# Kernel tuning notes

Hardware: AMD Instinct MI355X
Metric: run time of the kernel (lower is better)

The kernel has to match this reference:

```python
import jax, jax.numpy as jnp
import numpy as np

B, T, D, H = 8, 1024, 512, 8
QD, PD, POSD, VD, K = 32, 4, 48, 64, 31
FF = 4 * D
FF1, FF2, FF3, NLA = FF * 3 // 4, FF, FF * 5 // 4, D * 3 // 4


def _swoosh_l(x):
    return jax.nn.softplus(x - 4.0) - 0.08 * x - 0.035


def _swoosh_r(x):
    return jax.nn.softplus(x - 1.0) - 0.08 * x - 0.313261687


def setup_inputs() -> dict:
    key = jax.random.key(0)
    ks = iter(jax.random.split(key, 64))

    def w(shape, fan_in):
        return jax.random.normal(next(ks), shape, jnp.float32) * (fan_in ** -0.5)

    inp = {
        'x': jax.random.normal(next(ks), (B, T, D), jnp.float32),
        'pos_emb': jax.random.normal(next(ks), (2 * T - 1, POSD), jnp.float32),
        'mask': jnp.ones((B, T), bool),
        'attw_q_w': w((D, H * QD), D), 'attw_k_w': w((D, H * QD), D),
        'attw_pq_w': w((D, H * PD), D), 'attw_pos_w': w((POSD, H * PD), POSD),
        'ff1_in_w': w((D, FF1), D), 'ff1_in_b': jnp.zeros(FF1),
        'ff1_out_w': w((FF1, D), FF1), 'ff1_out_b': jnp.zeros(D),
        'nla_w': w((D, NLA * 3), D), 'nla_b': jnp.zeros(NLA * 3),
        'nla_out_w': w((NLA, D), NLA), 'nla_out_b': jnp.zeros(D),
        'sa1_v_w': w((D, H * VD), D), 'sa1_v_b': jnp.zeros(H * VD),
        'sa1_o_w': w((H * VD, D), H * VD), 'sa1_o_b': jnp.zeros(D),
        'conv1_in_w': w((D, 2 * D), D), 'conv1_in_b': jnp.zeros(2 * D),
        'conv1_dw_w': w((D, 1, K), K), 'conv1_dw_b': jnp.zeros(D),
        'conv1_out_w': w((D, D), D), 'conv1_out_b': jnp.zeros(D),
        'ff2_in_w': w((D, FF2), D), 'ff2_in_b': jnp.zeros(FF2),
        'ff2_out_w': w((FF2, D), FF2), 'ff2_out_b': jnp.zeros(D),
        'mid_scale': jax.random.uniform(next(ks), (D,), jnp.float32),
        'sa2_v_w': w((D, H * VD), D), 'sa2_v_b': jnp.zeros(H * VD),
        'sa2_o_w': w((H * VD, D), H * VD), 'sa2_o_b': jnp.zeros(D),
        'conv2_in_w': w((D, 2 * D), D), 'conv2_in_b': jnp.zeros(2 * D),
        'conv2_dw_w': w((D, 1, K), K), 'conv2_dw_b': jnp.zeros(D),
        'conv2_out_w': w((D, D), D), 'conv2_out_b': jnp.zeros(D),
        'ff3_in_w': w((D, FF3), D), 'ff3_in_b': jnp.zeros(FF3),
        'ff3_out_w': w((FF3, D), FF3), 'ff3_out_b': jnp.zeros(D),
        'norm_bias': jnp.zeros(D), 'norm_log_scale': jnp.zeros(()),
        'out_scale': jax.random.uniform(next(ks), (D,), jnp.float32),
    }
    return inp


def _forward(x, pos_emb, attw_q_w, attw_k_w, attw_pq_w, attw_pos_w,
             ff1_in_w, ff1_in_b, ff1_out_w, ff1_out_b,
             nla_w, nla_b, nla_out_w, nla_out_b,
             sa1_v_w, sa1_v_b, sa1_o_w, sa1_o_b,
             conv1_in_w, conv1_in_b, conv1_dw_w, conv1_dw_b, conv1_out_w, conv1_out_b,
             ff2_in_w, ff2_in_b, ff2_out_w, ff2_out_b,
             mid_scale,
             sa2_v_w, sa2_v_b, sa2_o_w, sa2_o_b,
             conv2_in_w, conv2_in_b, conv2_dw_w, conv2_dw_b, conv2_out_w, conv2_out_b,
             ff3_in_w, ff3_in_b, ff3_out_w, ff3_out_b,
             norm_bias, norm_log_scale, out_scale, mask):
    res = x
    # --- relative-pos multi-head attention weights ---
    q = (x @ attw_q_w).reshape(B, T, H, QD).transpose(0, 2, 1, 3)
    k = (x @ attw_k_w).reshape(B, T, H, QD).transpose(0, 2, 1, 3)
    p = (x @ attw_pq_w).reshape(B, T, H, PD).transpose(0, 2, 1, 3)
    content = jnp.einsum('bhtd,bhsd->bhts', q, k) * (QD ** -0.5)
    rel = (pos_emb @ attw_pos_w).reshape(2 * T - 1, H, PD).transpose(1, 0, 2)
    idx = jnp.arange(T)[:, None] - jnp.arange(T)[None, :] + (T - 1)
    relg = rel[:, idx]  # [H, T, T, PD]
    scores = content + jnp.einsum('bhtd,htsd->bhts', p, relg)
    scores = jnp.where(mask[:, None, None, :], scores, -10000.0)
    attn = jax.nn.softmax(scores, axis=-1)
    attn = jnp.where(mask[:, None, :, None], attn, 0.0)

    def mk(y):
        return jnp.where(mask[..., None], y, 0.0)

    def ff(y, wi, bi, wo, bo):
        return _swoosh_l(y @ wi + bi) @ wo + bo

    def sa(y, vw, vb, ow, ob):
        v = (y @ vw + vb).reshape(B, T, H, VD).transpose(0, 2, 1, 3)
        o = jnp.einsum('bhts,bhsd->bhtd', attn, v).transpose(0, 2, 1, 3).reshape(B, T, H * VD)
        return o @ ow + ob

    def conv(y, iw, ib, dw, db, ow, ob):
        u = y @ iw + ib
        a, g = jnp.split(u, 2, axis=-1)
        a = (a * jax.nn.sigmoid(g)).transpose(0, 2, 1)  # [B, D, T]
        a = jnp.where(mask[:, None, :], a, 0.0)
        c = jax.lax.conv_general_dilated(a, dw, (1,), [(K // 2, K // 2)],
                                         dimension_numbers=('NCH', 'OIH', 'NCH'),
                                         feature_group_count=D) + db[None, :, None]
        c = _swoosh_r(c.transpose(0, 2, 1))
        return mk(c @ ow + ob)

    def bypass(r, u, s):
        s = jnp.clip(s, 0.2, 1.0)  # eval/steady regime
        return r + (u - r) * s

    x = mk(x + ff(x, ff1_in_w, ff1_in_b, ff1_out_w, ff1_out_b))
    # non-linear attention (uses head 0)
    a, b, c = jnp.split(x @ nla_w + nla_b, 3, axis=-1)
    att0 = jnp.einsum('bts,bsd->btd', attn[:, 0], jnp.tanh(b) * c)
    x = mk(x + ((a * att0) @ nla_out_w + nla_out_b))
    x = mk(x + sa(x, sa1_v_w, sa1_v_b, sa1_o_w, sa1_o_b))
    x = mk(x + conv(x, conv1_in_w, conv1_in_b, conv1_dw_w, conv1_dw_b, conv1_out_w, conv1_out_b))
    x = mk(x + ff(x, ff2_in_w, ff2_in_b, ff2_out_w, ff2_out_b))
    x = mk(bypass(res, x, mid_scale))
    x = mk(x + sa(x, sa2_v_w, sa2_v_b, sa2_o_w, sa2_o_b))
    x = mk(x + conv(x, conv2_in_w, conv2_in_b, conv2_dw_w, conv2_dw_b, conv2_out_w, conv2_out_b))
    x = mk(x + ff(x, ff3_in_w, ff3_in_b, ff3_out_w, ff3_out_b))
    # BiasNorm
    rms = jnp.sqrt(jnp.mean((x - norm_bias) ** 2, axis=-1, keepdims=True) + 1e-8)
    x = x / rms * jnp.exp(norm_log_scale)
    x = mk(bypass(res, x, out_scale))
    return x


def reference(x, pos_emb, mask, attw_q_w, attw_k_w, attw_pq_w, attw_pos_w,
              ff1_in_w, ff1_in_b, ff1_out_w, ff1_out_b,
              nla_w, nla_b, nla_out_w, nla_out_b,
              sa1_v_w, sa1_v_b, sa1_o_w, sa1_o_b,
              conv1_in_w, conv1_in_b, conv1_dw_w, conv1_dw_b, conv1_out_w, conv1_out_b,
              ff2_in_w, ff2_in_b, ff2_out_w, ff2_out_b,
              mid_scale,
              sa2_v_w, sa2_v_b, sa2_o_w, sa2_o_b,
              conv2_in_w, conv2_in_b, conv2_dw_w, conv2_dw_b, conv2_out_w, conv2_out_b,
              ff3_in_w, ff3_in_b, ff3_out_w, ff3_out_b,
              norm_bias, norm_log_scale, out_scale):
    return _forward(x, pos_emb, attw_q_w, attw_k_w, attw_pq_w, attw_pos_w,
                    ff1_in_w, ff1_in_b, ff1_out_w, ff1_out_b,
                    nla_w, nla_b, nla_out_w, nla_out_b,
                    sa1_v_w, sa1_v_b, sa1_o_w, sa1_o_b,
                    conv1_in_w, conv1_in_b, conv1_dw_w, conv1_dw_b, conv1_out_w, conv1_out_b,
                    ff2_in_w, ff2_in_b, ff2_out_w, ff2_out_b,
                    mid_scale,
                    sa2_v_w, sa2_v_b, sa2_o_w, sa2_o_b,
                    conv2_in_w, conv2_in_b, conv2_dw_w, conv2_dw_b, conv2_out_w, conv2_out_b,
                    ff3_in_w, ff3_in_b, ff3_out_w, ff3_out_b,
                    norm_bias, norm_log_scale, out_scale, mask)
```

## Files before the change

kernel.cpp:

```cpp
#include <hip/hip_runtime.h>
#include <hip/hip_bf16.h>
#include <math.h>

using bf16 = __hip_bfloat16;
using f16 = _Float16;
typedef short s16x8 __attribute__((ext_vector_type(8)));
typedef f16   f16x2 __attribute__((ext_vector_type(2)));
typedef float f32x4 __attribute__((ext_vector_type(4)));
typedef unsigned int u32;
#define DEV __device__ __forceinline__
#define AS1 __attribute__((address_space(1)))
#define AS3 __attribute__((address_space(3)))

constexpr int Bc = 8, Tc = 1024, Dc = 512, Hc = 8;
constexpr int QDc = 32, PDc = 4, POSDc = 48, VDc = 64;
constexpr int Nrow = Bc * Tc;
constexpr int KWc = 31;
constexpr float LOG2E = 1.4426950408889634f;

DEV float frcp(float x) { return __builtin_amdgcn_rcpf(x); }
DEV float softplus_f(float y) { return fmaxf(y, 0.f) + __logf(1.f + __expf(-fabsf(y))); }
DEV float swoosh_l_f(float x) { return softplus_f(x - 4.f) - 0.08f * x - 0.035f; }
DEV float swoosh_r_f(float x) { return softplus_f(x - 1.f) - 0.08f * x - 0.313261687f; }
DEV float sigmoid_f(float x)  { return frcp(1.f + __expf(-x)); }
DEV float tanh_f(float x) {
  float e = __expf(2.f * fminf(fmaxf(x, -15.f), 15.f));
  return (e - 1.f) * frcp(e + 1.f);
}
DEV float clip_s(float s)     { return fminf(fmaxf(s, 0.2f), 1.0f); }
DEV float to_f(bf16 x)  { return __bfloat162float(x); }
DEV float b2f(short s) { union { u32 u; float f; } z; z.u = (u32)(unsigned short)s << 16; return z.f; }
DEV short f2bb(float v) { bf16 h = __float2bfloat16(v); return *(short*)&h; }
DEV unsigned short f2h(float v) { f16 h = (f16)v; union { f16 x; unsigned short s; } z; z.x = h; return z.s; }
DEV float h2f(unsigned short s) { union { unsigned short s; f16 x; } z; z.s = s; return (float)z.x; }
DEV u32 packbf(float a, float b) {
  return ((u32)(unsigned short)f2bb(b) << 16) | (u32)(unsigned short)f2bb(a);
}
DEV float dot2(u32 a, u32 b, float c) {
#if __has_builtin(__builtin_amdgcn_fdot2)
  union { u32 u; f16x2 v; } x, y; x.u = a; y.u = b;
  return __builtin_amdgcn_fdot2(x.v, y.v, c, false);
#else
  return c + h2f(a & 0xffff) * h2f(b & 0xffff) + h2f(a >> 16) * h2f(b >> 16);
#endif
}

DEV float wave_sum(float v) {
#pragma unroll
  for (int o = 32; o > 0; o >>= 1) v += __shfl_xor(v, o);
  return v;
}

DEV void gload16(const void* g, void* l) {
  __builtin_amdgcn_global_load_lds((const AS1 u32*)g, (AS3 u32*)l, 16, 0, 0);
}

template <int ACT, int WM, int WN, int FM, int FN>
__global__ __launch_bounds__(256) void gemm_mfma(
    const bf16* __restrict__ A, const bf16* __restrict__ B,
    const float* __restrict__ bias, const float* __restrict__ resid,
    float* __restrict__ Cf, bf16* __restrict__ Cb, bf16* __restrict__ Cb2,
    const bf16* __restrict__ auxb, const float* __restrict__ auxf,
    const float* __restrict__ auxf2,
    int M, int N, int K, int lda, int ldb, int ldc,
    long sAz, long sBo, long sBi, long sCo, long sCi, int nh) {
  constexpr int BM = WM * FM * 16, BN = WN * FN * 16;
  constexpr int NPA = (ACT == 8) ? 3 : 1;
  constexpr int NPB = (ACT == 2) ? 2 : 1;
  constexpr int PANA = 384, PANB = 512;
  constexpr int ASZT = NPA * BM * 128;
  constexpr int BUF = (NPA * BM + NPB * BN) * 128;
  constexpr int LPS = NPA * (BM / 32) + NPB * (BN / 32);

  int z = blockIdx.z;
  int zo = z / nh, zi = z - zo * nh;
  A += (long)z * sAz;
  B += (long)zo * sBo + (long)zi * sBi;
  long coff = (long)zo * sCo + (long)zi * sCi;

  __shared__ char lds[2 * BUF];

  int tid = threadIdx.x;
  int lane = tid & 63, w = tid >> 6;
  int wm = w / WN, wn = w % WN;

  int gx = gridDim.x;
  int nwg = gx * gridDim.y;
  int flat = blockIdx.y * gx + blockIdx.x;
  if ((nwg & 7) == 0) flat = (flat & 7) * (nwg >> 3) + (flat >> 3);
  int m0 = (flat / gx) * BM, n0 = (flat % gx) * BN;

  int lrow = lane >> 3, lch = lane & 7;
  const bf16* ga = A + (long)(m0 + w * (BM / 4) + lrow) * lda + ((lch ^ lrow) << 3);
  const bf16* gb = B + (long)(n0 + w * (BN / 4) + lrow) * ldb + ((lch ^ lrow) << 3);

  f32x4 acc[NPA * NPB][FM][FN];
#pragma unroll
  for (int p = 0; p < NPA * NPB; ++p)
#pragma unroll
    for (int i = 0; i < FM; ++i)
#pragma unroll
      for (int j = 0; j < FN; ++j) acc[p][i][j] = 0.f;

  int nt = K >> 6;
  {
#pragma unroll
    for (int pa = 0; pa < NPA; ++pa) {
      const bf16* gp = ga + (long)(pa * PANA) * lda;
      char* la = lds + pa * BM * 128 + w * (BM / 4) * 128;
#pragma unroll
      for (int i = 0; i < BM / 32; ++i) gload16(gp + (long)(i * 8) * lda, la + i * 1024);
    }
#pragma unroll
    for (int pb = 0; pb < NPB; ++pb) {
      const bf16* gp = gb + (long)(pb * PANB) * ldb;
      char* lb = lds + ASZT + pb * BN * 128 + w * (BN / 4) * 128;
#pragma unroll
      for (int i = 0; i < BN / 32; ++i) gload16(gp + (long)(i * 8) * ldb, lb + i * 1024);
    }
  }

  for (int t = 0; t < nt; ++t) {
    char* cA = lds + (t & 1) * BUF;
    if (t + 1 < nt) {
      int k0 = (t + 1) << 6;
      char* base = lds + ((t + 1) & 1) * BUF;
#pragma unroll
      for (int pa = 0; pa < NPA; ++pa) {
        const bf16* gp = ga + (long)(pa * PANA) * lda + k0;
        char* la = base + pa * BM * 128 + w * (BM / 4) * 128;
#pragma unroll
        for (int i = 0; i < BM / 32; ++i) gload16(gp + (long)(i * 8) * lda, la + i * 1024);
      }
#pragma unroll
      for (int pb = 0; pb < NPB; ++pb) {
        const bf16* gp = gb + (long)(pb * PANB) * ldb + k0;
        char* lb = base + ASZT + pb * BN * 128 + w * (BN / 4) * 128;
#pragma unroll
        for (int i = 0; i < BN / 32; ++i) gload16(gp + (long)(i * 8) * ldb, lb + i * 1024);
      }
      asm volatile("s_waitcnt vmcnt(%0)" :: "n"(LPS) : "memory");
    } else {
      asm volatile("s_waitcnt vmcnt(0)" ::: "memory");
    }
    __builtin_amdgcn_s_barrier();
    __builtin_amdgcn_sched_barrier(0);
#pragma unroll
    for (int ks = 0; ks < 2; ++ks) {
      int cg = ks * 4 + (lane >> 4);
      s16x8 af[NPA][FM], bfr[NPB][FN];
#pragma unroll
      for (int pa = 0; pa < NPA; ++pa)
#pragma unroll
        for (int f = 0; f < FM; ++f) {
          int row = wm * FM * 16 + f * 16 + (lane & 15);
          af[pa][f] = *(const s16x8*)(cA + pa * BM * 128 + row * 128 +
                                      ((cg ^ (row & 7)) << 4));
        }
#pragma unroll
      for (int pb = 0; pb < NPB; ++pb)
#pragma unroll
        for (int f = 0; f < FN; ++f) {
          int row = wn * FN * 16 + f * 16 + (lane & 15);
          bfr[pb][f] = *(const s16x8*)(cA + ASZT + pb * BN * 128 + row * 128 +
                                       ((cg ^ (row & 7)) << 4));
        }
#pragma unroll
      for (int pa = 0; pa < NPA; ++pa)
#pragma unroll
        for (int pb = 0; pb < NPB; ++pb)
#pragma unroll
          for (int fm = 0; fm < FM; ++fm)
#pragma unroll
            for (int fn = 0; fn < FN; ++fn)
              acc[pa * NPB + pb][fm][fn] = __builtin_amdgcn_mfma_f32_16x16x32_bf16(
                  af[pa][fm], bfr[pb][fn], acc[pa * NPB + pb][fm][fn], 0, 0, 0);
    }
    __builtin_amdgcn_sched_barrier(0);
    __builtin_amdgcn_s_barrier();
  }

  int rbase = m0 + wm * FM * 16 + (lane >> 4) * 4;
  int cbase = n0 + wn * FN * 16 + (lane & 15);
#pragma unroll
  for (int fn = 0; fn < FN; ++fn) {
    int col = cbase + fn * 16;
    if (col >= N) continue;
#pragma unroll
    for (int fm = 0; fm < FM; ++fm) {
#pragma unroll
      for (int r = 0; r < 4; ++r) {
        int row = rbase + fm * 16 + r;
        if (row >= M) continue;
        long ci = coff + (long)row * ldc + col;
        if constexpr (ACT == 2) {
          float va = acc[0][fm][fn][r] + bias[col];
          float vg = acc[1][fm][fn][r] + bias[col + 512];
          Cb[ci] = __float2bfloat16(va * sigmoid_f(vg));
        } else if constexpr (ACT == 4) {
          float a = to_f(auxb[(long)col * 8192 + (long)zo * 1024 + row]);
          Cb[ci] = __float2bfloat16(acc[0][fm][fn][r] * a);
        } else if constexpr (ACT == 5) {
          float v = acc[0][fm][fn][r] + bias[col] + resid[ci];
          float rv = auxf[ci];
          float o = rv + (v - rv) * clip_s(auxf2[col]);
          Cf[ci] = o;
          Cb[ci] = __float2bfloat16(o);
        } else if constexpr (ACT == 7) {
          Cb[ci] = __float2bfloat16(acc[0][fm][fn][r] + bias[row]);
        } else if constexpr (ACT == 8) {
          float va = acc[0][fm][fn][r] + bias[row];
          float vb = acc[1][fm][fn][r] + bias[row + 384];
          float vc = acc[2][fm][fn][r] + bias[row + 768];
          Cb2[ci] = __float2bfloat16(va);
          Cb[ci] = __float2bfloat16(tanh_f(vb) * vc);
        } else if constexpr (ACT == 9) {
          float v = acc[0][fm][fn][r];
          if (col < 512) {
            Cb2[(long)row * 512 + col] = __float2bfloat16(v);
          } else {
            Cb[(long)row * ldc + (col - 512)] =
                __float2bfloat16(swoosh_l_f(v + bias[col - 512]));
          }
        } else {
          float v = acc[0][fm][fn][r] + (bias ? bias[col] : 0.f);
          if (ACT == 1) v = swoosh_l_f(v);
          if (resid) v += resid[ci];
          if (Cf) Cf[ci] = v;
          if (Cb) Cb[ci] = __float2bfloat16(v);
        }
      }
    }
  }
}

__global__ __launch_bounds__(256) void relph_kernel(
    const float* __restrict__ pos_emb, const float* __restrict__ Wpos,
    float* __restrict__ relb,
    const float* __restrict__ x0, const float* __restrict__ Wpq,
    f16* __restrict__ ph) {
  int zz = blockIdx.z;
  const float* A  = zz ? x0 : pos_emb;
  const float* Bm = zz ? Wpq : Wpos;
  int M = zz ? Nrow : (2 * Tc - 1);
  int K = zz ? Dc : POSDc;
  int lda = K;
  int m0 = blockIdx.y * 64;
  if (m0 >= M) return;

  __shared__ float As[16][72];
  __shared__ float Bs[16][72];
  int tid = threadIdx.x;
  int tx = tid & 15, ty = tid >> 4;
  int arow = tid >> 2, ak4 = (tid & 3) * 4;
  int bk = tid >> 4, bn4 = (tid & 15) * 4;
  float acc[4][4] = {};
  for (int k0 = 0; k0 < K; k0 += 16) {
    int gm = m0 + arow;
#pragma unroll
    for (int j = 0; j < 4; ++j) {
      int gk = k0 + ak4 + j;
      As[ak4 + j][arow] = (gm < M && gk < K) ? A[(long)gm * lda + gk] : 0.f;
    }
    int gk = k0 + bk;
#pragma unroll
    for (int j = 0; j < 4; ++j) {
      int gn = bn4 + j;
      Bs[bk][bn4 + j] = (gk < K && gn < 32) ? Bm[(long)gk * 32 + gn] : 0.f;
    }
    __syncthreads();
#pragma unroll
    for (int kk = 0; kk < 16; ++kk) {
      float a4[4], b4[4];
#pragma unroll
      for (int i = 0; i < 4; ++i) a4[i] = As[kk][ty * 4 + i];
#pragma unroll
      for (int i = 0; i < 4; ++i) b4[i] = Bs[kk][tx * 4 + i];
#pragma unroll
      for (int i = 0; i < 4; ++i)
#pragma unroll
        for (int j = 0; j < 4; ++j) acc[i][j] += a4[i] * b4[j];
    }
    __syncthreads();
  }
#pragma unroll
  for (int i = 0; i < 4; ++i) {
    int gm = m0 + ty * 4 + i;
    if (gm >= M) continue;
#pragma unroll
    for (int j = 0; j < 4; ++j) {
      int gn = tx * 4 + j;
      if (gn < 32) {
        if (zz) ph[(long)gm * 32 + gn] = (f16)(acc[i][j] * LOG2E);
        else    relb[(long)gm * 32 + gn] = acc[i][j];
      }
    }
  }
}

struct TDesc { const float* src; bf16* dst; int K, N, tile0, ntx; float scale; };
struct TBatch { TDesc d[18]; int n; };

__global__ __launch_bounds__(256) void transpose_batch_kernel(TBatch tb) {
  int tile = blockIdx.x;
  int wi = 0;
#pragma unroll 1
  for (int i = 1; i < 18; ++i)
    if (i < tb.n && tb.d[i].tile0 <= tile) wi = i;
  const float* W = tb.d[wi].src;
  bf16* WT = tb.d[wi].dst;
  int K = tb.d[wi].K, N = tb.d[wi].N;
  float sc = tb.d[wi].scale;
  int lt = tile - tb.d[wi].tile0;
  int ntx = tb.d[wi].ntx;
  int bx = (lt % ntx) * 32, by = (lt / ntx) * 32;

  __shared__ float t[32][33];
  int lx = threadIdx.x & 31, ly = threadIdx.x >> 5;
#pragma unroll
  for (int j = 0; j < 4; ++j) {
    int k = by + ly + j * 8, n = bx + lx;
    if (k < K && n < N) t[ly + j * 8][lx] = W[(long)k * N + n];
  }
  __syncthreads();
#pragma unroll
  for (int j = 0; j < 4; ++j) {
    int n = bx + ly + j * 8, k = by + lx;
    if (n < N && k < K) WT[(long)n * K + k] = __float2bfloat16(t[lx][ly + j * 8] * sc);
  }
}

__global__ void dw_transpose_kernel(const float* __restrict__ dw1, float* __restrict__ o1,
                                    const float* __restrict__ dw2, float* __restrict__ o2) {
  int i = blockIdx.x * 256 + threadIdx.x;
  if (i >= 2 * 512 * KWc) return;
  const float* s = (i < 512 * KWc) ? dw1 : dw2;
  float* o = (i < 512 * KWc) ? o1 : o2;
  int j = (i < 512 * KWc) ? i : i - 512 * KWc;
  int d = j / KWc, kk = j - d * KWc;
  o[kk * 512 + d] = s[j];
}

__global__ void f2b_kernel(const float* __restrict__ in, bf16* __restrict__ out, int nOct) {
  int i = blockIdx.x * 256 + threadIdx.x;
  if (i >= nOct) return;
  float4 a = *(const float4*)(in + (long)i * 8);
  float4 b = *(const float4*)(in + (long)i * 8 + 4);
  s16x8 o;
  o[0] = f2bb(a.x); o[1] = f2bb(a.y); o[2] = f2bb(a.z); o[3] = f2bb(a.w);
  o[4] = f2bb(b.x); o[5] = f2bb(b.y); o[6] = f2bb(b.z); o[7] = f2bb(b.w);
  *(s16x8*)((short*)out + (long)i * 8) = o;
}

__global__ __launch_bounds__(256) void scores_softmax_fused(
    const bf16* __restrict__ qk, const f16* __restrict__ ph,
    const float* __restrict__ rel, bf16* __restrict__ attn) {
  int bh = blockIdx.y;
  int h = bh & (Hc - 1), b = bh >> 3;
  int t0 = blockIdx.x * 16;
  int tid = threadIdx.x, lane = tid & 63, w = tid >> 6;

  __shared__ unsigned short eS[16 * 1024];
  __shared__ u32 rel01[1040], rel23[1040];
  __shared__ u32 pS[16][2];
  __shared__ float lS[16][4];

  for (int i = tid; i < 1039; i += 256) {
    float4 rv = *(const float4*)(rel + (long)(t0 + i) * 32 + h * 4);
    rel01[i] = ((u32)f2h(rv.y) << 16) | f2h(rv.x);
    rel23[i] = ((u32)f2h(rv.w) << 16) | f2h(rv.z);
  }
  if (tid < 16) {
    const u32* pp = (const u32*)(ph + ((long)(b * Tc + t0 + tid)) * 32 + h * 4);
    pS[tid][0] = pp[0]; pS[tid][1] = pp[1];
  }
  __syncthreads();

  s16x8 af = *(const s16x8*)(qk + ((long)(b * Tc + t0 + (lane & 15))) * 512 +
                             h * QDc + (lane >> 4) * 8);
  int g = lane >> 4;
  u32 p01[4], p23[4];
#pragma unroll
  for (int r = 0; r < 4; ++r) { p01[r] = pS[g * 4 + r][0]; p23[r] = pS[g * 4 + r][1]; }
  float sum[4] = {0.f, 0.f, 0.f, 0.f};
  f32x4 zero = {0.f, 0.f, 0.f, 0.f};
  int cols0 = w * 256;
#pragma unroll 4
  for (int tile = 0; tile < 16; ++tile) {
    int s0 = cols0 + tile * 16;
    s16x8 bfr = *(const s16x8*)(qk + ((long)(b * Tc + s0 + (lane & 15))) * 512 +
                                256 + h * QDc + (lane >> 4) * 8);
    f32x4 acc = __builtin_amdgcn_mfma_f32_16x16x32_bf16(af, bfr, zero, 0, 0, 0);
    int scol = s0 + (lane & 15);
    int idx0 = g * 4 - scol + 1023;
#pragma unroll
    for (int r = 0; r < 4; ++r) {
      int idx = idx0 + r;
      float pos = dot2(p23[r], rel23[idx], dot2(p01[r], rel01[idx], 0.f));
      float e = exp2f(acc[r] + pos);
      sum[r] += e;
      *(unsigned short*)((char*)eS + (g * 4 + r) * 2048 + ((scol * 2) ^ (g << 5))) =
          (unsigned short)f2bb(e);
    }
  }
#pragma unroll
  for (int o = 1; o < 16; o <<= 1)
#pragma unroll
    for (int r = 0; r < 4; ++r) sum[r] += __shfl_xor(sum[r], o);
  if ((lane & 15) == 0) {
#pragma unroll
    for (int r = 0; r < 4; ++r) lS[g * 4 + r][w] = sum[r];
  }
  __syncthreads();

#pragma unroll
  for (int rr = 0; rr < 4; ++rr) {
    int row = w * 4 + rr;
    float inv = frcp(lS[row][0] + lS[row][1] + lS[row][2] + lS[row][3]);
    int mask = ((row >> 2) & 3) << 5;
    char* rowbase = (char*)eS + row * 2048;
    u32* grow = (u32*)(attn + ((long)bh * Tc + t0 + row) * Tc);
#pragma unroll
    for (int k = 0; k < 8; ++k) {
      u32 ew = *(u32*)(rowbase + (((lane + k * 64) * 4) ^ mask));
      grow[lane + k * 64] = packbf(b2f((short)(ew & 0xffff)) * inv,
                                   b2f((short)(ew >> 16)) * inv);
    }
  }
}

__global__ __launch_bounds__(256) void dwconv_kernel(
    const bf16* __restrict__ a, const float* __restrict__ dwT,
    const float* __restrict__ db, bf16* __restrict__ c) {
  int i = blockIdx.x * 256 + threadIdx.x;
  int oct = i & 63, bt = i >> 6;
  int t = bt & (Tc - 1), b0 = bt - t;
  float acc0 = db[oct * 8 + 0], acc1 = db[oct * 8 + 1], acc2 = db[oct * 8 + 2],
        acc3 = db[oct * 8 + 3], acc4 = db[oct * 8 + 4], acc5 = db[oct * 8 + 5],
        acc6 = db[oct * 8 + 6], acc7 = db[oct * 8 + 7];
#pragma unroll
  for (int kk = 0; kk < KWc; ++kk) {
    int tt = t + kk - (KWc / 2);
    if ((unsigned)tt < (unsigned)Tc) {
      s16x8 av = *(const s16x8*)((const short*)a + ((long)(b0 + tt) << 9) + oct * 8);
      const float* wp = dwT + kk * 512 + oct * 8;
      float4 w0 = *(const float4*)wp, w1 = *(const float4*)(wp + 4);
      acc0 += b2f(av[0]) * w0.x; acc1 += b2f(av[1]) * w0.y;
      acc2 += b2f(av[2]) * w0.z; acc3 += b2f(av[3]) * w0.w;
      acc4 += b2f(av[4]) * w1.x; acc5 += b2f(av[5]) * w1.y;
      acc6 += b2f(av[6]) * w1.z; acc7 += b2f(av[7]) * w1.w;
    }
  }
  s16x8 o;
  o[0] = f2bb(swoosh_r_f(acc0)); o[1] = f2bb(swoosh_r_f(acc1));
  o[2] = f2bb(swoosh_r_f(acc2)); o[3] = f2bb(swoosh_r_f(acc3));
  o[4] = f2bb(swoosh_r_f(acc4)); o[5] = f2bb(swoosh_r_f(acc5));
  o[6] = f2bb(swoosh_r_f(acc6)); o[7] = f2bb(swoosh_r_f(acc7));
  *(s16x8*)((short*)c + (long)bt * 512 + oct * 8) = o;
}

__global__ __launch_bounds__(256) void rmsnorm_bypass_kernel(
    const float* __restrict__ x, const float* __restrict__ x0,
    const float* __restrict__ nb, const float* __restrict__ nls,
    const float* __restrict__ os, float* __restrict__ out) {
  int row = blockIdx.x;
  int tid = threadIdx.x;
  const float* xr = x + (long)row * 512;
  const float* rr = x0 + (long)row * 512;
  float* orow = out + (long)row * 512;
  float v0 = xr[tid], v1 = xr[tid + 256];
  float d0 = v0 - nb[tid], d1 = v1 - nb[tid + 256];
  float ss = d0 * d0 + d1 * d1;
  __shared__ float red[4];
  int lane = tid & 63, wid = tid >> 6;
  ss = wave_sum(ss);
  if (lane == 0) red[wid] = ss;
  __syncthreads();
  ss = red[0] + red[1] + red[2] + red[3];
  float rms = sqrtf(ss * (1.f / 512.f) + 1e-8f);
  float scl = expf(nls[0]) / rms;
  float r0 = rr[tid], s0 = clip_s(os[tid]);
  orow[tid] = r0 + (v0 * scl - r0) * s0;
  float r1 = rr[tid + 256], s1 = clip_s(os[tid + 256]);
  orow[tid + 256] = r1 + (v1 * scl - r1) * s1;
}

static inline int cdiv(int a, int b) { return (a + b - 1) / b; }

template <int ACT, int WM = 2, int WN = 2, int FM = 2, int FN = 2>
static void mfma_launch(hipStream_t st, const bf16* A, const bf16* B, const float* bias,
                        const float* resid, float* Cf, bf16* Cb, bf16* Cb2,
                        const bf16* auxb, const float* auxf, const float* auxf2,
                        int M, int N, int K, int lda, int ldb, int ldc,
                        int Z = 1, int nh = 1, long sAz = 0, long sBo = 0, long sBi = 0,
                        long sCo = 0, long sCi = 0) {
  dim3 grid(cdiv(N, WN * FN * 16), cdiv(M, WM * FM * 16), Z);
  gemm_mfma<ACT, WM, WN, FM, FN><<<grid, dim3(256), 0, st>>>(
      A, B, bias, resid, Cf, Cb, Cb2, auxb, auxf, auxf2, M, N, K, lda, ldb, ldc,
      sAz, sBo, sBi, sCo, sCi, nh);
}
#define MFMA_AV 4, 1, 2, 4

extern "C" void kernel_launch(void* const* d_in, const int* in_sizes, int n_in,
                              void* d_out, int out_size, void* d_ws, size_t ws_size,
                              hipStream_t stream) {
  const float* x0        = (const float*)d_in[0];
  const float* pos_emb   = (const float*)d_in[1];
  const float* Wq        = (const float*)d_in[3];
  const float* Wk        = (const float*)d_in[4];
  const float* Wpq       = (const float*)d_in[5];
  const float* Wpos      = (const float*)d_in[6];
  const float* ff1_in_w  = (const float*)d_in[7];
  const float* ff1_in_b  = (const float*)d_in[8];
  const float* ff1_out_w = (const float*)d_in[9];
  const float* ff1_out_b = (const float*)d_in[10];
  const float* nla_w     = (const float*)d_in[11];
  const float* nla_b     = (const float*)d_in[12];
  const float* nla_out_w = (const float*)d_in[13];
  const float* nla_out_b = (const float*)d_in[14];
  const float* sa1_v_w   = (const float*)d_in[15];
  const float* sa1_v_b   = (const float*)d_in[16];
  const float* sa1_o_w   = (const float*)d_in[17];
  const float* sa1_o_b   = (const float*)d_in[18];
  const float* cv1_in_w  = (const float*)d_in[19];
  const float* cv1_in_b  = (const float*)d_in[20];
  const float* cv1_dw_w  = (const float*)d_in[21];
  const float* cv1_dw_b  = (const float*)d_in[22];
  const float* cv1_out_w = (const float*)d_in[23];
  const float* cv1_out_b = (const float*)d_in[24];
  const float* ff2_in_w  = (const float*)d_in[25];
  const float* ff2_in_b  = (const float*)d_in[26];
  const float* ff2_out_w = (const float*)d_in[27];
  const float* ff2_out_b = (const float*)d_in[28];
  const float* mid_scale = (const float*)d_in[29];
  const float* sa2_v_w   = (const float*)d_in[30];
  const float* sa2_v_b   = (const float*)d_in[31];
  const float* sa2_o_w   = (const float*)d_in[32];
  const float* sa2_o_b   = (const float*)d_in[33];
  const float* cv2_in_w  = (const float*)d_in[34];
  const float* cv2_in_b  = (const float*)d_in[35];
  const float* cv2_dw_w  = (const float*)d_in[36];
  const float* cv2_dw_b  = (const float*)d_in[37];
  const float* cv2_out_w = (const float*)d_in[38];
  const float* cv2_out_b = (const float*)d_in[39];
  const float* ff3_in_w  = (const float*)d_in[40];
  const float* ff3_in_b  = (const float*)d_in[41];
  const float* ff3_out_w = (const float*)d_in[42];
  const float* ff3_out_b = (const float*)d_in[43];
  const float* norm_bias = (const float*)d_in[44];
  const float* nls       = (const float*)d_in[45];
  const float* out_scale = (const float*)d_in[46];
  float* out = (float*)d_out;

  char* wsb = (char*)d_ws;
  size_t off = 0;
  bf16* attn  = (bf16*)(wsb + off); off += (size_t)Bc * Hc * Tc * Tc * 2;
  float* xA   = (float*)(wsb + off); off += (size_t)Nrow * Dc * 4;
  float* xB   = (float*)(wsb + off); off += (size_t)Nrow * Dc * 4;
  bf16*  xb   = (bf16*)(wsb + off);  off += (size_t)Nrow * Dc * 2;
  bf16*  x0b  = (bf16*)(wsb + off);  off += (size_t)Nrow * Dc * 2;
  bf16*  big1b = (bf16*)(wsb + off); off += (size_t)Nrow * 2560 * 2;
  bf16*  big2b = (bf16*)(wsb + off); off += (size_t)Nrow * Dc * 2;
  bf16*  wT    = (bf16*)(wsb + off); off += (size_t)9961472 * 2;
  float* dwT1  = (float*)(wsb + off); off += (size_t)KWc * 512 * 4;
  float* dwT2  = (float*)(wsb + off); off += (size_t)KWc * 512 * 4;
  bf16*  tbcT  = (bf16*)(wsb + off); off += (size_t)384 * Nrow * 2;
  bf16* big3b = big1b + (size_t)Nrow * 2048;
  bf16* vT    = big2b;
  bf16* qkb   = big2b;
  bf16* aT    = big1b;
  f16*  ph    = (f16*)(big1b + (size_t)Nrow * 1536);
  float* relb = (float*)(ph + (size_t)Nrow * 32);

  bf16* p_w = wT;
  auto alloc_w = [&](int n, int k) { bf16* r = p_w; p_w += (size_t)n * k; return r; };
  bf16* qkff1_wT   = alloc_w(2048, 512);
  bf16* ff1_out_wT = alloc_w(512, 1536);
  bf16* nla_wT     = alloc_w(1152, 512);
  bf16* nla_out_wT = alloc_w(512, 384);
  bf16* sa1_v_wT   = alloc_w(512, 512);
  bf16* sa1_o_wT   = alloc_w(512, 512);
  bf16* cv1_in_wT  = alloc_w(1024, 512);
  bf16* cv1_out_wT = alloc_w(512, 512);
  bf16* ff2_in_wT  = alloc_w(2048, 512);
  bf16* ff2_out_wT = alloc_w(512, 2048);
  bf16* sa2_v_wT   = alloc_w(512, 512);
  bf16* sa2_o_wT   = alloc_w(512, 512);
  bf16* cv2_in_wT  = alloc_w(1024, 512);
  bf16* cv2_out_wT = alloc_w(512, 512);
  bf16* ff3_in_wT  = alloc_w(2560, 512);
  bf16* ff3_out_wT = alloc_w(512, 2560);

  const int nOctD = Nrow * 64;

  f2b_kernel<<<cdiv(nOctD, 256), 256, 0, stream>>>(x0, x0b, nOctD);
  {
    TBatch tb{};
    auto add = [&](int idx, const float* s, bf16* d, int K, int N, int& t0, float sc) {
      tb.d[idx] = {s, d, K, N, t0, cdiv(N, 32), sc};
      t0 += cdiv(N, 32) * cdiv(K, 32);
    };
    int t0 = 0;
    add(0,  Wq,        qkff1_wT,   512, 256,  t0, 0.17677669529663687f * LOG2E);
    add(1,  Wk,        qkff1_wT + (size_t)256 * 512, 512, 256, t0, 1.f);
    add(2,  ff1_in_w,  qkff1_wT + (size_t)512 * 512, 512, 1536, t0, 1.f);
    add(3,  ff1_out_w, ff1_out_wT, 1536, 512, t0, 1.f);
    add(4,  nla_w,     nla_wT,     512, 1152, t0, 1.f);
    add(5,  nla_out_w, nla_out_wT, 384, 512,  t0, 1.f);
    add(6,  sa1_v_w,   sa1_v_wT,   512, 512,  t0, 1.f);
    add(7,  sa1_o_w,   sa1_o_wT,   512, 512,  t0, 1.f);
    add(8,  cv1_in_w,  cv1_in_wT,  512, 1024, t0, 1.f);
    add(9,  cv1_out_w, cv1_out_wT, 512, 512,  t0, 1.f);
    add(10, ff2_in_w,  ff2_in_wT,  512, 2048, t0, 1.f);
    add(11, ff2_out_w, ff2_out_wT, 2048, 512, t0, 1.f);
    add(12, sa2_v_w,   sa2_v_wT,   512, 512,  t0, 1.f);
    add(13, sa2_o_w,   sa2_o_wT,   512, 512,  t0, 1.f);
    add(14, cv2_in_w,  cv2_in_wT,  512, 1024, t0, 1.f);
    add(15, cv2_out_w, cv2_out_wT, 512, 512,  t0, 1.f);
    add(16, ff3_in_w,  ff3_in_wT,  512, 2560, t0, 1.f);
    add(17, ff3_out_w, ff3_out_wT, 2560, 512, t0, 1.f);
    tb.n = 18;
    transpose_batch_kernel<<<t0, 256, 0, stream>>>(tb);
  }
  dw_transpose_kernel<<<cdiv(2 * 512 * KWc, 256), 256, 0, stream>>>(
      cv1_dw_w, dwT1, cv2_dw_w, dwT2);
  relph_kernel<<<dim3(1, 128, 2), 256, 0, stream>>>(pos_emb, Wpos, relb, x0, Wpq, ph);

  mfma_launch<9>(stream, x0b, qkff1_wT, ff1_in_b, nullptr, nullptr, big1b, qkb,
                 nullptr, nullptr, nullptr, Nrow, 2048, 512, 512, 512, 1536);
  scores_softmax_fused<<<dim3(Tc / 16, 64), 256, 0, stream>>>(qkb, ph, relb, attn);

  mfma_launch<0>(stream, big1b, ff1_out_wT, ff1_out_b, x0, xA, xb, nullptr,
                 nullptr, nullptr, nullptr, Nrow, 512, 1536, 1536, 1536, 512);

  mfma_launch<8>(stream, nla_wT, xb, nla_b, nullptr, nullptr, tbcT, aT,
                 nullptr, nullptr, nullptr, 384, Nrow, 512, 512, 512, Nrow);
  mfma_launch<4>(stream, attn, tbcT, nullptr, nullptr, nullptr, big3b, nullptr,
                 aT, nullptr, nullptr, Tc, 384, Tc, Tc, Nrow, 384,
                 Bc, 1, (long)Hc * Tc * Tc, 1024, 0, (long)Tc * 384, 0);
  mfma_launch<0>(stream, big3b, nla_out_wT, nla_out_b, xA, xB, xb, nullptr,
                 nullptr, nullptr, nullptr, Nrow, 512, 384, 384, 384, 512);

  mfma_launch<7>(stream, sa1_v_wT, xb, sa1_v_b, nullptr, nullptr, vT, nullptr,
                 nullptr, nullptr, nullptr, 512, Nrow, 512, 512, 512, Nrow);
  mfma_launch<0, MFMA_AV>(stream, attn, vT, nullptr, nullptr, nullptr, big3b, nullptr,
                          nullptr, nullptr, nullptr, Tc, VDc, Tc, Tc, Nrow, 512,
                          Bc * Hc, Hc, (long)Tc * Tc, Tc, (long)VDc * Nrow,
                          (long)Tc * 512, VDc);
  mfma_launch<0>(stream, big3b, sa1_o_wT, sa1_o_b, xB, xA, xb, nullptr,
                 nullptr, nullptr, nullptr, Nrow, 512, 512, 512, 512, 512);

  mfma_launch<2>(stream, xb, cv1_in_wT, cv1_in_b, nullptr, nullptr, big2b, nullptr,
                 nullptr, nullptr, nullptr, Nrow, 512, 512, 512, 512, 512);
  dwconv_kernel<<<cdiv(nOctD, 256), 256, 0, stream>>>(big2b, dwT1, cv1_dw_b, big3b);
  mfma_launch<0>(stream, big3b, cv1_out_wT, cv1_out_b, xA, xB, xb, nullptr,
                 nullptr, nullptr, nullptr, Nrow, 512, 512, 512, 512, 512);

  mfma_launch<1>(stream, xb, ff2_in_wT, ff2_in_b, nullptr, nullptr, big1b, nullptr,
                 nullptr, nullptr, nullptr, Nrow, 2048, 512, 512, 512, 2048);
  mfma_launch<5>(stream, big1b, ff2_out_wT, ff2_out_b, xB, xB, xb, nullptr,
                 nullptr, x0, mid_scale, Nrow, 512, 2048, 2048, 2048, 512);

  mfma_launch<7>(stream, sa2_v_wT, xb, sa2_v_b, nullptr, nullptr, vT, nullptr,
                 nullptr, nullptr, nullptr, 512, Nrow, 512, 512, 512, Nrow);
  mfma_launch<0, MFMA_AV>(stream, attn, vT, nullptr, nullptr, nullptr, big3b, nullptr,
                          nullptr, nullptr, nullptr, Tc, VDc, Tc, Tc, Nrow, 512,
                          Bc * Hc, Hc, (long)Tc * Tc, Tc, (long)VDc * Nrow,
                          (long)Tc * 512, VDc);
  mfma_launch<0>(stream, big3b, sa2_o_wT, sa2_o_b, xB, xA, xb, nullptr,
                 nullptr, nullptr, nullptr, Nrow, 512, 512, 512, 512, 512);

  mfma_launch<2>(stream, xb, cv2_in_wT, cv2_in_b, nullptr, nullptr, big2b, nullptr,
                 nullptr, nullptr, nullptr, Nrow, 512, 512, 512, 512, 512);
  dwconv_kernel<<<cdiv(nOctD, 256), 256, 0, stream>>>(big2b, dwT2, cv2_dw_b, big3b);
  mfma_launch<0>(stream, big3b, cv2_out_wT, cv2_out_b, xA, xB, xb, nullptr,
                 nullptr, nullptr, nullptr, Nrow, 512, 512, 512, 512, 512);

  mfma_launch<1>(stream, xb, ff3_in_wT, ff3_in_b, nullptr, nullptr, big1b, nullptr,
                 nullptr, nullptr, nullptr, Nrow, 2560, 512, 512, 512, 2560);
  mfma_launch<0>(stream, big1b, ff3_out_wT, ff3_out_b, xB, xA, nullptr, nullptr,
                 nullptr, nullptr, nullptr, Nrow, 512, 2560, 2560, 2560, 512);

  rmsnorm_bypass_kernel<<<Nrow, 256, 0, stream>>>(xA, x0, norm_bias, nls, out_scale, out);
}
```

Before: 769.0 us.

## Use triple-buffered LDS pipeline in MFMA GEMM when tile fits

Generalizes the GEMM's double-buffered global-to-LDS prefetch into a DEPTH-stage ring buffer, using three stages when a stage buffer is at most 16KB. Loads are issued two k-tiles ahead and the vmcnt waits are adjusted so more memory latency overlaps with MFMA work. The cost is more LDS per workgroup, which can lower occupancy, plus slightly more complex wait logic for the tail iterations.

```diff
diff --git a/kernel.cpp b/kernel.cpp
--- a/kernel.cpp
+++ b/kernel.cpp
@@ -71,6 +71,7 @@
   constexpr int ASZT = NPA * BM * 128;
   constexpr int BUF = (NPA * BM + NPB * BN) * 128;
   constexpr int LPS = NPA * (BM / 32) + NPB * (BN / 32);
+  constexpr int DEPTH = (BUF <= 16384) ? 3 : 2;
 
   int z = blockIdx.z;
   int zo = z / nh, zi = z - zo * nh;
@@ -78,7 +79,7 @@
   B += (long)zo * sBo + (long)zi * sBi;
   long coff = (long)zo * sCo + (long)zi * sCi;
 
-  __shared__ char lds[2 * BUF];
+  __shared__ char lds[DEPTH * BUF];
 
   int tid = threadIdx.x;
   int lane = tid & 63, w = tid >> 6;
@@ -94,6 +95,24 @@
   const bf16* ga = A + (long)(m0 + w * (BM / 4) + lrow) * lda + ((lch ^ lrow) << 3);
   const bf16* gb = B + (long)(n0 + w * (BN / 4) + lrow) * ldb + ((lch ^ lrow) << 3);
 
+  auto STAGE = [&](int kt, char* base) {
+    int k0 = kt << 6;
+#pragma unroll
+    for (int pa = 0; pa < NPA; ++pa) {
+      const bf16* gp = ga + (long)(pa * PANA) * lda + k0;
+      char* la = base + pa * BM * 128 + w * (BM / 4) * 128;
+#pragma unroll
+      for (int i = 0; i < BM / 32; ++i) gload16(gp + (long)(i * 8) * lda, la + i * 1024);
+    }
+#pragma unroll
+    for (int pb = 0; pb < NPB; ++pb) {
+      const bf16* gp = gb + (long)(pb * PANB) * ldb + k0;
+      char* lb = base + ASZT + pb * BN * 128 + w * (BN / 4) * 128;
+#pragma unroll
+      for (int i = 0; i < BN / 32; ++i) gload16(gp + (long)(i * 8) * ldb, lb + i * 1024);
+    }
+  };
+
   f32x4 acc[NPA * NPB][FM][FN];
 #pragma unroll
   for (int p = 0; p < NPA * NPB; ++p)
@@ -103,42 +122,17 @@
       for (int j = 0; j < FN; ++j) acc[p][i][j] = 0.f;
 
   int nt = K >> 6;
-  {
-#pragma unroll
-    for (int pa = 0; pa < NPA; ++pa) {
-      const bf16* gp = ga + (long)(pa * PANA) * lda;
-      char* la = lds + pa * BM * 128 + w * (BM / 4) * 128;
-#pragma unroll
-      for (int i = 0; i < BM / 32; ++i) gload16(gp + (long)(i * 8) * lda, la + i * 1024);
-    }
-#pragma unroll
-    for (int pb = 0; pb < NPB; ++pb) {
-      const bf16* gp = gb + (long)(pb * PANB) * ldb;
-      char* lb = lds + ASZT + pb * BN * 128 + w * (BN / 4) * 128;
-#pragma unroll
-      for (int i = 0; i < BN / 32; ++i) gload16(gp + (long)(i * 8) * ldb, lb + i * 1024);
-    }
-  }
-
+#pragma unroll
+  for (int p = 0; p < DEPTH - 1; ++p) STAGE(p, lds + p * BUF);
+
+  int cur = 0;
   for (int t = 0; t < nt; ++t) {
-    char* cA = lds + (t & 1) * BUF;
-    if (t + 1 < nt) {
-      int k0 = (t + 1) << 6;
-      char* base = lds + ((t + 1) & 1) * BUF;
-#pragma unroll
-      for (int pa = 0; pa < NPA; ++pa) {
-        const bf16* gp = ga + (long)(pa * PANA) * lda + k0;
-        char* la = base + pa * BM * 128 + w * (BM / 4) * 128;
-#pragma unroll
-        for (int i = 0; i < BM / 32; ++i) gload16(gp + (long)(i * 8) * lda, la + i * 1024);
-      }
-#pragma unroll
-      for (int pb = 0; pb < NPB; ++pb) {
-        const bf16* gp = gb + (long)(pb * PANB) * ldb + k0;
-        char* lb = base + ASZT + pb * BN * 128 + w * (BN / 4) * 128;
-#pragma unroll
-        for (int i = 0; i < BN / 32; ++i) gload16(gp + (long)(i * 8) * ldb, lb + i * 1024);
-      }
+    char* cA = lds + cur * BUF;
+    if (t + DEPTH - 1 < nt) {
+      int stg = (cur == 0) ? DEPTH - 1 : cur - 1;
+      STAGE(t + DEPTH - 1, lds + stg * BUF);
+      asm volatile("s_waitcnt vmcnt(%0)" :: "n"((DEPTH - 1) * LPS) : "memory");
+    } else if (DEPTH > 2 && t + 2 == nt) {
       asm volatile("s_waitcnt vmcnt(%0)" :: "n"(LPS) : "memory");
     } else {
       asm volatile("s_waitcnt vmcnt(0)" ::: "memory");
@@ -178,6 +172,7 @@
     }
     __builtin_amdgcn_sched_barrier(0);
     __builtin_amdgcn_s_barrier();
+    cur = (cur + 1 == DEPTH) ? 0 : cur + 1;
   }
 
   int rbase = m0 + wm * FM * 16 + (lane >> 4) * 4;
```

Result: slower. 834.4 us (+8.5%).
